# Optimization experiments

Hardware: AMD Instinct MI355X
Metric: run time of the kernel (lower is better)

The kernel has to match this reference:

```python
import jax, jax.numpy as jnp
import numpy as np
import math

B, S, D = 16, 2048, 128
MASK_SENTINEL = -100

def setup_inputs() -> dict:
    key = jax.random.key(0)
    k1, k2, k3, k4 = jax.random.split(key, 4)
    value = jax.random.normal(k1, (B, S, D), dtype=jnp.float32)
    key_t = jax.random.normal(k2, (B, S, D), dtype=jnp.float32)
    query = jax.random.normal(k3, (B, S, D), dtype=jnp.float32)
    # mask uses -100 as the "masked out" sentinel, anything else is kept.
    bits = jax.random.randint(k4, (B, S, S), 0, 2, dtype=jnp.int32)
    mask = jnp.where(bits == 0, jnp.int32(MASK_SENTINEL), jnp.int32(0))
    return {"value": value, "key": key_t, "query": query, "mask": mask}

def reference(value, key, query, mask):
    # scores: [B, Sq, Sk]
    scale = 1.0 / math.sqrt(query.shape[-1])
    scores = jnp.einsum("bqd,bkd->bqk", query, key) * scale
    min_val = jnp.finfo(scores.dtype).min
    masked = jnp.where(mask == MASK_SENTINEL, min_val, scores)
    attn = jax.nn.softmax(masked, axis=-1)
    return jnp.einsum("bqk,bkd->bqd", attn, value)
```

## Files before the change

### kernel.cpp

```cpp
#include <hip/hip_runtime.h>
#include <hip/hip_bf16.h>

#define BATCH 16
#define SEQ   2048
#define DIM   128
#define QBLK  64
#define KVBLK 64
#define NT    (SEQ / KVBLK)
#define PPAD  72
#define L2E   1.4426950408889634f
#define THR   8.0f
#define MSENT -100

typedef __attribute__((ext_vector_type(8))) short bf16x8;
typedef __attribute__((ext_vector_type(4))) float f32x4;
typedef __attribute__((ext_vector_type(4))) int   i32x4;
typedef __attribute__((ext_vector_type(4))) unsigned u32x4;

__device__ __forceinline__ unsigned short f2bf(float f) {
  union { float f; unsigned u; } v; v.f = f;
  return (unsigned short)((v.u + 0x7FFFu + ((v.u >> 16) & 1u)) >> 16);
}
__device__ __forceinline__ unsigned packbf(float a, float b) {
  return ((unsigned)f2bf(b) << 16) | (unsigned)f2bf(a);
}

__global__ __launch_bounds__(256) void cvt_k(const float* __restrict__ K,
                                             short* __restrict__ Kb) {
  const size_t i = ((size_t)blockIdx.x * 256 + threadIdx.x) * 8;
  f32x4 a = __builtin_nontemporal_load((const f32x4*)(K + i));
  f32x4 b = __builtin_nontemporal_load((const f32x4*)(K + i + 4));
  u32x4 o = { packbf(a[0], a[1]), packbf(a[2], a[3]),
              packbf(b[0], b[1]), packbf(b[2], b[3]) };
  *(u32x4*)(Kb + i) = o;
}

__global__ __launch_bounds__(256) void cvt_vt(const float* __restrict__ V,
                                              short* __restrict__ Vt) {
  __shared__ unsigned t32[64][65];
  const int tid = threadIdx.x;
  const int b  = blockIdx.x >> 5;
  const int s0 = (blockIdx.x & 31) * 64;
  #pragma unroll
  for (int it = 0; it < 8; ++it) {
    const int idx = tid + it * 256;
    const int r = idx >> 5, c4 = idx & 31;
    f32x4 x = __builtin_nontemporal_load(
        (const f32x4*)(V + ((size_t)b * SEQ + s0 + r) * DIM + c4 * 4));
    t32[r][c4 * 2]     = packbf(x[0], x[1]);
    t32[r][c4 * 2 + 1] = packbf(x[2], x[3]);
  }
  __syncthreads();
  const int d = tid >> 1, sh = tid & 1;
  unsigned short outv[32];
  #pragma unroll
  for (int j = 0; j < 32; ++j) {
    const unsigned u = t32[sh * 32 + j][d >> 1];
    outv[j] = (d & 1) ? (unsigned short)(u >> 16) : (unsigned short)(u & 0xffff);
  }
  short* op = Vt + ((size_t)b * DIM + d) * SEQ + s0 + sh * 32;
  #pragma unroll
  for (int q = 0; q < 4; ++q) {
    bf16x8 y;
    #pragma unroll
    for (int j = 0; j < 8; ++j) y[j] = (short)outv[q * 8 + j];
    *(bf16x8*)(op + q * 8) = y;
  }
}

__device__ __forceinline__ void gload16(const void* g, void* l) {
  __builtin_amdgcn_global_load_lds(
      (const __attribute__((address_space(1))) unsigned*)g,
      (__attribute__((address_space(3))) unsigned*)l, 16, 0, 0);
}

__device__ __forceinline__ void stage_k(const char* __restrict__ Kb2,
                                        int k0, int w, int l, void* kbuf) {
  #pragma unroll
  for (int it = 0; it < 4; ++it) {
    const int ch = w * 4 + it;
    const int r  = ch * 4 + (l >> 4);
    const int sg = (l & 15) ^ (r & 15);
    gload16(Kb2 + (size_t)(k0 + r) * 256 + sg * 16, (char*)kbuf + ch * 1024);
  }
}
__device__ __forceinline__ void stage_v(const char* __restrict__ Vtb2,
                                        int k0, int w, int l, void* vbuf) {
  #pragma unroll
  for (int it = 0; it < 4; ++it) {
    const int ch = w * 4 + it;
    const int d2 = ch * 4 + (l >> 4);
    const int Su = (l & 15) ^ (d2 & 15);
    const int d  = 2 * d2 + (Su >> 3);
    const int m  = Su & 7;
    gload16(Vtb2 + (size_t)d * (SEQ * 2) + (size_t)k0 * 2 + m * 16,
            (char*)vbuf + ch * 1024);
  }
}

#define TILE_BODY(T, PAR, SA, SB, MA, MB)                                      \
  {                                                                            \
    if ((T) + 2 < NT) stage_k(Kb2, ((T) + 2) * KVBLK, w, l, lds_k[(PAR)]);     \
    if ((T) + 1 < NT) {                                                        \
      stage_v(Vtb2, ((T) + 1) * KVBLK, w, l, lds_v[(PAR) ^ 1]);                \
      _Pragma("unroll") for (int sub = 0; sub < 4; ++sub)                      \
          MB[sub] = __builtin_nontemporal_load(                                \
              (const i32x4*)(Mr + ((T) + 1) * KVBLK + 16 * sub + 4 * g));      \
    }                                                                          \
    __builtin_amdgcn_sched_barrier(0);                                         \
                  \
    _Pragma("unroll") for (int sub = 0; sub < 4; ++sub)                        \
        _Pragma("unroll") for (int i = 0; i < 4; ++i)                          \
            if (MA[sub][i] == MSENT) SA[sub][i] = -1e30f;                      \
    {                                                                          \
      float tm = -1e30f;                                                       \
      _Pragma("unroll") for (int sub = 0; sub < 4; ++sub)                      \
          _Pragma("unroll") for (int i = 0; i < 4; ++i)                        \
              tm = fmaxf(tm, SA[sub][i]);                                      \
      tm = fmaxf(tm, __shfl_xor(tm, 16));                                      \
      tm = fmaxf(tm, __shfl_xor(tm, 32));                                      \
      if (__any(tm > mrow + THR)) {                                            \
        const float mnew = fmaxf(mrow, tm);                                    \
        const float al = __builtin_amdgcn_exp2f((mrow - mnew) * L2E);          \
        mrow = mnew; lsum *= al;                                               \
        float av[4];                                                           \
        _Pragma("unroll") for (int i = 0; i < 4; ++i)                          \
            av[i] = __shfl(al, 4 * g + i);                                     \
        _Pragma("unroll") for (int t8 = 0; t8 < 8; ++t8)                       \
            _Pragma("unroll") for (int i = 0; i < 4; ++i)                      \
                acc[t8][i] *= av[i];                                           \
      }                                                                        \
    }                                                                          \
               \
    if ((T) + 1 < NT) {                                                        \
      const char* kb_ = (const char*)lds_k[(PAR) ^ 1];                         \
      _Pragma("unroll") for (int sub = 0; sub < 4; ++sub)                      \
          SB[sub] = (f32x4){0.f, 0.f, 0.f, 0.f};                               \
      __builtin_amdgcn_s_setprio(1);                                           \
      _Pragma("unroll") for (int kk = 0; kk < 4; ++kk) {                       \
        const int cb = (64 * kk + 16 * g) ^ (lr << 4);                         \
        _Pragma("unroll") for (int sub = 0; sub < 4; ++sub) {                  \
          bf16x8 kb = *(const bf16x8*)(kb_ + (sub * 16 + lr) * 256 + cb);      \
          SB[sub] = __builtin_amdgcn_mfma_f32_16x16x32_bf16(kb, qa[kk],        \
                                                            SB[sub], 0, 0, 0); \
        }                                                                      \
      }                                                                        \
      __builtin_amdgcn_s_setprio(0);                                           \
    }                                                                          \
                               \
    {                                                                          \
      unsigned* prow = (unsigned*)&lds_p[w][lr * PPAD];                        \
      _Pragma("unroll") for (int sub = 0; sub < 4; ++sub) {                    \
        const float p0 = __builtin_amdgcn_exp2f((SA[sub][0] - mrow) * L2E);    \
        const float p1 = __builtin_amdgcn_exp2f((SA[sub][1] - mrow) * L2E);    \
        const float p2 = __builtin_amdgcn_exp2f((SA[sub][2] - mrow) * L2E);    \
        const float p3 = __builtin_amdgcn_exp2f((SA[sub][3] - mrow) * L2E);    \
        lsum += (p0 + p1) + (p2 + p3);                                         \
        prow[8 * sub + 2 * g]     = packbf(p0, p1);                            \
        prow[8 * sub + 2 * g + 1] = packbf(p2, p3);                            \
      }                                                                        \
      bf16x8 pa0 = *(const bf16x8*)&lds_p[w][lr * PPAD + g * 8];               \
      bf16x8 pa1 = *(const bf16x8*)&lds_p[w][lr * PPAD + 32 + g * 8];          \
      const char* vb_ = (const char*)lds_v[(PAR)];                             \
      __builtin_amdgcn_s_setprio(1);                                           \
      _Pragma("unroll") for (int t8 = 0; t8 < 8; ++t8) {                       \
        const int d2 = 8 * t8 + (lr >> 1);                                     \
        const int S0 = (((lr & 1) * 8 + 0 + g) ^ (d2 & 15)) * 16;              \
        const int S1 = (((lr & 1) * 8 + 4 + g) ^ (d2 & 15)) * 16;              \
        bf16x8 v0 = *(const bf16x8*)(vb_ + d2 * 256 + S0);                     \
        acc[t8] = __builtin_amdgcn_mfma_f32_16x16x32_bf16(pa0, v0, acc[t8],    \
                                                          0, 0, 0);            \
        bf16x8 v1 = *(const bf16x8*)(vb_ + d2 * 256 + S1);                     \
        acc[t8] = __builtin_amdgcn_mfma_f32_16x16x32_bf16(pa1, v1, acc[t8],    \
                                                          0, 0, 0);            \
      }                                                                        \
      __builtin_amdgcn_s_setprio(0);                                           \
    }                                                                          \
    if ((T) + 1 < NT) __syncthreads();                                         \
  }

__global__ __launch_bounds__(256, 2) void attn_fwd(
    const short* __restrict__ Kbf, const short* __restrict__ Vt,
    const float* __restrict__ Qg, const int* __restrict__ Mg,
    float* __restrict__ Og) {
  __shared__ short lds_k[2][KVBLK * DIM];
  __shared__ short lds_v[2][DIM * KVBLK];
  __shared__ short lds_p[4][16 * PPAD];

  const int tid = threadIdx.x;
  const int w = tid >> 6, l = tid & 63, g = l >> 4, lr = l & 15;

  const int blk = blockIdx.x;
  const int swz = (blk & 7) * 64 + (blk >> 3);
  const int b   = swz >> 5;
  const int q0  = (swz & 31) * QBLK;

  const float scale = 0.08838834764831845f;

  const char* Kb2  = (const char*)(Kbf + (size_t)b * SEQ * DIM);
  const char* Vtb2 = (const char*)(Vt  + (size_t)b * DIM * SEQ);
  const int*  Mr   = Mg + (size_t)b * SEQ * SEQ + (size_t)(q0 + w * 16 + lr) * SEQ;

  stage_k(Kb2, 0,     w, l, lds_k[0]);
  stage_k(Kb2, KVBLK, w, l, lds_k[1]);
  stage_v(Vtb2, 0,    w, l, lds_v[0]);
  __builtin_amdgcn_sched_barrier(0);
  i32x4 mA[4], mB[4];
  #pragma unroll
  for (int sub = 0; sub < 4; ++sub)
    mA[sub] = __builtin_nontemporal_load((const i32x4*)(Mr + 16 * sub + 4 * g));

  bf16x8 qa[4];
  {
    const float* qbase = Qg + ((size_t)b * SEQ + (size_t)(q0 + w * 16 + lr)) * DIM + g * 8;
    #pragma unroll
    for (int kk = 0; kk < 4; ++kk) {
      f32x4 x0 = *(const f32x4*)(qbase + kk * 32);
      f32x4 x1 = *(const f32x4*)(qbase + kk * 32 + 4);
      bf16x8 f;
      #pragma unroll
      for (int j = 0; j < 4; ++j) {
        f[j]     = (short)f2bf(x0[j] * scale);
        f[j + 4] = (short)f2bf(x1[j] * scale);
      }
      qa[kk] = f;
    }
  }

  f32x4 acc[8];
  #pragma unroll
  for (int t = 0; t < 8; ++t) acc[t] = (f32x4){0.f, 0.f, 0.f, 0.f};
  float mrow = -1e30f, lsum = 0.f;

  __syncthreads();

  f32x4 sA[4], sB[4];
  #pragma unroll
  for (int sub = 0; sub < 4; ++sub) sA[sub] = (f32x4){0.f, 0.f, 0.f, 0.f};
  {
    const char* kb_ = (const char*)lds_k[0];
    #pragma unroll
    for (int kk = 0; kk < 4; ++kk) {
      const int cb = (64 * kk + 16 * g) ^ (lr << 4);
      #pragma unroll
      for (int sub = 0; sub < 4; ++sub) {
        bf16x8 kb = *(const bf16x8*)(kb_ + (sub * 16 + lr) * 256 + cb);
        sA[sub] = __builtin_amdgcn_mfma_f32_16x16x32_bf16(kb, qa[kk], sA[sub], 0, 0, 0);
      }
    }
  }
  __syncthreads();

  for (int t = 0; t < NT; t += 2) {
    TILE_BODY(t,     0, sA, sB, mA, mB);
    TILE_BODY(t + 1, 1, sB, sA, mB, mA);
  }

  lsum += __shfl_xor(lsum, 16);
  lsum += __shfl_xor(lsum, 32);
  const float rden = 1.f / lsum;
  float rdv[4];
  #pragma unroll
  for (int i = 0; i < 4; ++i) rdv[i] = __shfl(rden, 4 * g + i);
  float* ob = Og + ((size_t)b * SEQ + (size_t)(q0 + w * 16)) * DIM;
  #pragma unroll
  for (int t8 = 0; t8 < 8; ++t8)
    #pragma unroll
    for (int i = 0; i < 4; ++i)
      ob[(4 * g + i) * DIM + 16 * t8 + lr] = acc[t8][i] * rdv[i];
}

extern "C" void kernel_launch(void* const* d_in, const int* in_sizes, int n_in,
                              void* d_out, int out_size, void* d_ws, size_t ws_size,
                              hipStream_t stream) {
  (void)in_sizes; (void)n_in; (void)out_size; (void)ws_size;
  const float* Vg = (const float*)d_in[0];
  const float* Kg = (const float*)d_in[1];
  const float* Qg = (const float*)d_in[2];
  const int*   Mg = (const int*)d_in[3];
  float* Og = (float*)d_out;

  short* Kbf = (short*)d_ws;
  short* Vt  = Kbf + (size_t)BATCH * SEQ * DIM;
  cvt_k<<<dim3(BATCH * SEQ * DIM / (8 * 256)), 256, 0, stream>>>(Kg, Kbf);
  cvt_vt<<<dim3(BATCH * (SEQ / 64)), 256, 0, stream>>>(Vg, Vt);
  attn_fwd<<<dim3(BATCH * (SEQ / QBLK)), 256, 0, stream>>>(Kbf, Vt, Qg, Mg, Og);
}
```

Measured before the change: 109.0 us.

## Shrink KV tile to 32, triple-buffer K/V, pass P via shuffles instead of LDS

```diff
diff --git a/kernel.cpp b/kernel.cpp
--- a/kernel.cpp
+++ b/kernel.cpp
@@ -5,9 +5,8 @@
 #define SEQ   2048
 #define DIM   128
 #define QBLK  64
-#define KVBLK 64
-#define NT    (SEQ / KVBLK)
-#define PPAD  72
+#define KVB   32
+#define NT    (SEQ / KVB)
 #define L2E   1.4426950408889634f
 #define THR   8.0f
 #define MSENT -100
@@ -74,49 +73,47 @@
       (__attribute__((address_space(3))) unsigned*)l, 16, 0, 0);
 }
 
-__device__ __forceinline__ void stage_k(const char* __restrict__ Kb2,
-                                        int k0, int w, int l, void* kbuf) {
-  #pragma unroll
-  for (int it = 0; it < 4; ++it) {
-    const int ch = w * 4 + it;
+__device__ __forceinline__ void stage_k32(const char* __restrict__ Kb2,
+                                          int k0, int w, int l, void* kbuf) {
+  #pragma unroll
+  for (int it = 0; it < 2; ++it) {
+    const int ch = w * 2 + it;
     const int r  = ch * 4 + (l >> 4);
     const int sg = (l & 15) ^ (r & 15);
     gload16(Kb2 + (size_t)(k0 + r) * 256 + sg * 16, (char*)kbuf + ch * 1024);
   }
 }
-__device__ __forceinline__ void stage_v(const char* __restrict__ Vtb2,
-                                        int k0, int w, int l, void* vbuf) {
-  #pragma unroll
-  for (int it = 0; it < 4; ++it) {
-    const int ch = w * 4 + it;
-    const int d2 = ch * 4 + (l >> 4);
-    const int Su = (l & 15) ^ (d2 & 15);
-    const int d  = 2 * d2 + (Su >> 3);
-    const int m  = Su & 7;
-    gload16(Vtb2 + (size_t)d * (SEQ * 2) + (size_t)k0 * 2 + m * 16,
+__device__ __forceinline__ void stage_v32(const char* __restrict__ Vtb2,
+                                          int k0, int w, int l, void* vbuf) {
+  #pragma unroll
+  for (int it = 0; it < 2; ++it) {
+    const int ch = w * 2 + it;
+    const int d  = ch * 16 + (l >> 2);
+    const int sp = (l & 3) ^ ((l >> 3) & 3);
+    gload16(Vtb2 + (size_t)d * (SEQ * 2) + (size_t)k0 * 2 + sp * 16,
             (char*)vbuf + ch * 1024);
   }
 }
 
-#define TILE_BODY(T, PAR, SA, SB, MA, MB)                                      \
+#define TILE_BODY(T, SA, SB, MA, MB, BARMODE)                                  \
   {                                                                            \
-    if ((T) + 2 < NT) stage_k(Kb2, ((T) + 2) * KVBLK, w, l, lds_k[(PAR)]);     \
+    if ((T) + 3 < NT) stage_k32(Kb2, ((T) + 3) * KVB, w, l, kA);               \
+    if ((T) + 2 < NT) stage_v32(Vtb2, ((T) + 2) * KVB, w, l, vC);              \
     if ((T) + 1 < NT) {                                                        \
-      stage_v(Vtb2, ((T) + 1) * KVBLK, w, l, lds_v[(PAR) ^ 1]);                \
-      _Pragma("unroll") for (int sub = 0; sub < 4; ++sub)                      \
-          MB[sub] = __builtin_nontemporal_load(                                \
-              (const i32x4*)(Mr + ((T) + 1) * KVBLK + 16 * sub + 4 * g));      \
+      MB[0] = __builtin_nontemporal_load(                                      \
+          (const i32x4*)(Mr + ((T) + 1) * KVB + 4 * g));                       \
+      MB[1] = __builtin_nontemporal_load(                                      \
+          (const i32x4*)(Mr + ((T) + 1) * KVB + 16 + 4 * g));                  \
     }                                                                          \
     __builtin_amdgcn_sched_barrier(0);                                         \
                   \
-    _Pragma("unroll") for (int sub = 0; sub < 4; ++sub)                        \
+    _Pragma("unroll") for (int sub = 0; sub < 2; ++sub)                        \
         _Pragma("unroll") for (int i = 0; i < 4; ++i)                          \
             if (MA[sub][i] == MSENT) SA[sub][i] = -1e30f;                      \
     {                                                                          \
-      float tm = -1e30f;                                                       \
-      _Pragma("unroll") for (int sub = 0; sub < 4; ++sub)                      \
-          _Pragma("unroll") for (int i = 0; i < 4; ++i)                        \
-              tm = fmaxf(tm, SA[sub][i]);                                      \
+      float tm = fmaxf(fmaxf(SA[0][0], SA[0][1]), fmaxf(SA[0][2], SA[0][3])); \
+      tm = fmaxf(tm, fmaxf(fmaxf(SA[1][0], SA[1][1]),                          \
+                           fmaxf(SA[1][2], SA[1][3])));                        \
       tm = fmaxf(tm, __shfl_xor(tm, 16));                                      \
       tm = fmaxf(tm, __shfl_xor(tm, 32));                                      \
       if (__any(tm > mrow + THR)) {                                            \
@@ -131,61 +128,76 @@
                 acc[t8][i] *= av[i];                                           \
       }                                                                        \
     }                                                                          \
-               \
+                       \
     if ((T) + 1 < NT) {                                                        \
-      const char* kb_ = (const char*)lds_k[(PAR) ^ 1];                         \
-      _Pragma("unroll") for (int sub = 0; sub < 4; ++sub)                      \
-          SB[sub] = (f32x4){0.f, 0.f, 0.f, 0.f};                               \
+      SB[0] = (f32x4){0.f, 0.f, 0.f, 0.f};                                     \
+      SB[1] = (f32x4){0.f, 0.f, 0.f, 0.f};                                     \
       __builtin_amdgcn_s_setprio(1);                                           \
       _Pragma("unroll") for (int kk = 0; kk < 4; ++kk) {                       \
         const int cb = (64 * kk + 16 * g) ^ (lr << 4);                         \
-        _Pragma("unroll") for (int sub = 0; sub < 4; ++sub) {                  \
-          bf16x8 kb = *(const bf16x8*)(kb_ + (sub * 16 + lr) * 256 + cb);      \
-          SB[sub] = __builtin_amdgcn_mfma_f32_16x16x32_bf16(kb, qa[kk],        \
-                                                            SB[sub], 0, 0, 0); \
-        }                                                                      \
+        bf16x8 kb0 = *(const bf16x8*)(kB + lr * 256 + cb);                     \
+        bf16x8 kb1 = *(const bf16x8*)(kB + (16 + lr) * 256 + cb);              \
+        SB[0] = __builtin_amdgcn_mfma_f32_16x16x32_bf16(kb0, qa[kk], SB[0],    \
+                                                        0, 0, 0);              \
+        SB[1] = __builtin_amdgcn_mfma_f32_16x16x32_bf16(kb1, qa[kk], SB[1],    \
+                                                        0, 0, 0);              \
       }                                                                        \
       __builtin_amdgcn_s_setprio(0);                                           \
     }                                                                          \
-                               \
+      \
     {                                                                          \
-      unsigned* prow = (unsigned*)&lds_p[w][lr * PPAD];                        \
-      _Pragma("unroll") for (int sub = 0; sub < 4; ++sub) {                    \
+      unsigned pk[2][2];                                                       \
+      _Pragma("unroll") for (int sub = 0; sub < 2; ++sub) {                    \
         const float p0 = __builtin_amdgcn_exp2f((SA[sub][0] - mrow) * L2E);    \
         const float p1 = __builtin_amdgcn_exp2f((SA[sub][1] - mrow) * L2E);    \
         const float p2 = __builtin_amdgcn_exp2f((SA[sub][2] - mrow) * L2E);    \
         const float p3 = __builtin_amdgcn_exp2f((SA[sub][3] - mrow) * L2E);    \
         lsum += (p0 + p1) + (p2 + p3);                                         \
-        prow[8 * sub + 2 * g]     = packbf(p0, p1);                            \
-        prow[8 * sub + 2 * g + 1] = packbf(p2, p3);                            \
-      }                                                                        \
-      bf16x8 pa0 = *(const bf16x8*)&lds_p[w][lr * PPAD + g * 8];               \
-      bf16x8 pa1 = *(const bf16x8*)&lds_p[w][lr * PPAD + 32 + g * 8];          \
-      const char* vb_ = (const char*)lds_v[(PAR)];                             \
+        pk[sub][0] = packbf(p0, p1);                                           \
+        pk[sub][1] = packbf(p2, p3);                                           \
+      }                                                                        \
+      const unsigned s00 = (unsigned)__shfl((int)pk[0][0], laneA);             \
+      const unsigned s01 = (unsigned)__shfl((int)pk[0][1], laneA);             \
+      const unsigned s02 = (unsigned)__shfl((int)pk[0][0], laneB);             \
+      const unsigned s03 = (unsigned)__shfl((int)pk[0][1], laneB);             \
+      const unsigned s10 = (unsigned)__shfl((int)pk[1][0], laneA);             \
+      const unsigned s11 = (unsigned)__shfl((int)pk[1][1], laneA);             \
+      const unsigned s12 = (unsigned)__shfl((int)pk[1][0], laneB);             \
+      const unsigned s13 = (unsigned)__shfl((int)pk[1][1], laneB);             \
+      const bool hi = (g >= 2);                                                \
+      union { unsigned u[4]; bf16x8 v; } pa;                                   \
+      pa.u[0] = hi ? s10 : s00;                                                \
+      pa.u[1] = hi ? s11 : s01;                                                \
+      pa.u[2] = hi ? s12 : s02;                                                \
+      pa.u[3] = hi ? s13 : s03;                                                \
+      const int Sv = ((g ^ ((lr >> 1) & 3)) << 4);                             \
       __builtin_amdgcn_s_setprio(1);                                           \
       _Pragma("unroll") for (int t8 = 0; t8 < 8; ++t8) {                       \
-        const int d2 = 8 * t8 + (lr >> 1);                                     \
-        const int S0 = (((lr & 1) * 8 + 0 + g) ^ (d2 & 15)) * 16;              \
-        const int S1 = (((lr & 1) * 8 + 4 + g) ^ (d2 & 15)) * 16;              \
-        bf16x8 v0 = *(const bf16x8*)(vb_ + d2 * 256 + S0);                     \
-        acc[t8] = __builtin_amdgcn_mfma_f32_16x16x32_bf16(pa0, v0, acc[t8],    \
+        bf16x8 vb = *(const bf16x8*)(vA + (16 * t8 + lr) * 64 + Sv);           \
+        acc[t8] = __builtin_amdgcn_mfma_f32_16x16x32_bf16(pa.v, vb, acc[t8],   \
                                                           0, 0, 0);            \
-        bf16x8 v1 = *(const bf16x8*)(vb_ + d2 * 256 + S1);                     \
-        acc[t8] = __builtin_amdgcn_mfma_f32_16x16x32_bf16(pa1, v1, acc[t8],    \
-                                                          0, 0, 0);            \
       }                                                                        \
       __builtin_amdgcn_s_setprio(0);                                           \
     }                                                                          \
-    if ((T) + 1 < NT) __syncthreads();                                         \
+    if ((T) + 1 < NT) {                                                        \
+      if (BARMODE) {                                                           \
+        __syncthreads();                                                       \
+      } else {                                                                 \
+        asm volatile("s_waitcnt vmcnt(6)" ::: "memory");                       \
+        __builtin_amdgcn_s_barrier();                                          \
+        __builtin_amdgcn_sched_barrier(0);                                     \
+      }                                                                        \
+    }                                                                          \
+    { char* t_ = kA; kA = kB; kB = kC; kC = t_; }                              \
+    { char* t_ = vA; vA = vB; vB = vC; vC = t_; }                              \
   }
 
 __global__ __launch_bounds__(256, 2) void attn_fwd(
     const short* __restrict__ Kbf, const short* __restrict__ Vt,
     const float* __restrict__ Qg, const int* __restrict__ Mg,
     float* __restrict__ Og) {
-  __shared__ short lds_k[2][KVBLK * DIM];
-  __shared__ short lds_v[2][DIM * KVBLK];
-  __shared__ short lds_p[4][16 * PPAD];
+  __shared__ short lds_k[3][KVB * DIM];
+  __shared__ short lds_v[3][DIM * KVB];
 
   const int tid = threadIdx.x;
   const int w = tid >> 6, l = tid & 63, g = l >> 4, lr = l & 15;
@@ -201,14 +213,18 @@
   const char* Vtb2 = (const char*)(Vt  + (size_t)b * DIM * SEQ);
   const int*  Mr   = Mg + (size_t)b * SEQ * SEQ + (size_t)(q0 + w * 16 + lr) * SEQ;
 
-  stage_k(Kb2, 0,     w, l, lds_k[0]);
-  stage_k(Kb2, KVBLK, w, l, lds_k[1]);
-  stage_v(Vtb2, 0,    w, l, lds_v[0]);
+  char *kA = (char*)lds_k[0], *kB = (char*)lds_k[1], *kC = (char*)lds_k[2];
+  char *vA = (char*)lds_v[0], *vB = (char*)lds_v[1], *vC = (char*)lds_v[2];
+
+  stage_k32(Kb2, 0,       w, l, kA);
+  stage_k32(Kb2, KVB,     w, l, kB);
+  stage_k32(Kb2, 2 * KVB, w, l, kC);
+  stage_v32(Vtb2, 0,      w, l, vA);
+  stage_v32(Vtb2, KVB,    w, l, vB);
   __builtin_amdgcn_sched_barrier(0);
-  i32x4 mA[4], mB[4];
-  #pragma unroll
-  for (int sub = 0; sub < 4; ++sub)
-    mA[sub] = __builtin_nontemporal_load((const i32x4*)(Mr + 16 * sub + 4 * g));
+  i32x4 mA[2], mB[2];
+  mA[0] = __builtin_nontemporal_load((const i32x4*)(Mr + 4 * g));
+  mA[1] = __builtin_nontemporal_load((const i32x4*)(Mr + 16 + 4 * g));
 
   bf16x8 qa[4];
   {
@@ -232,29 +248,32 @@
   for (int t = 0; t < 8; ++t) acc[t] = (f32x4){0.f, 0.f, 0.f, 0.f};
   float mrow = -1e30f, lsum = 0.f;
 
+  const int laneA = ((g & 1) << 5) + lr;
+  const int laneB = laneA + 16;
+
   __syncthreads();
 
-  f32x4 sA[4], sB[4];
-  #pragma unroll
-  for (int sub = 0; sub < 4; ++sub) sA[sub] = (f32x4){0.f, 0.f, 0.f, 0.f};
-  {
-    const char* kb_ = (const char*)lds_k[0];
-    #pragma unroll
-    for (int kk = 0; kk < 4; ++kk) {
-      const int cb = (64 * kk + 16 * g) ^ (lr << 4);
-      #pragma unroll
-      for (int sub = 0; sub < 4; ++sub) {
-        bf16x8 kb = *(const bf16x8*)(kb_ + (sub * 16 + lr) * 256 + cb);
-        sA[sub] = __builtin_amdgcn_mfma_f32_16x16x32_bf16(kb, qa[kk], sA[sub], 0, 0, 0);
-      }
-    }
+  f32x4 sA[2], sB[2];
+  sA[0] = (f32x4){0.f, 0.f, 0.f, 0.f};
+  sA[1] = (f32x4){0.f, 0.f, 0.f, 0.f};
+  #pragma unroll
+  for (int kk = 0; kk < 4; ++kk) {
+    const int cb = (64 * kk + 16 * g) ^ (lr << 4);
+    bf16x8 kb0 = *(const bf16x8*)(kA + lr * 256 + cb);
+    bf16x8 kb1 = *(const bf16x8*)(kA + (16 + lr) * 256 + cb);
+    sA[0] = __builtin_amdgcn_mfma_f32_16x16x32_bf16(kb0, qa[kk], sA[0], 0, 0, 0);
+    sA[1] = __builtin_amdgcn_mfma_f32_16x16x32_bf16(kb1, qa[kk], sA[1], 0, 0, 0);
   }
   __syncthreads();
 
-  for (int t = 0; t < NT; t += 2) {
-    TILE_BODY(t,     0, sA, sB, mA, mB);
-    TILE_BODY(t + 1, 1, sB, sA, mB, mA);
-  }
+  for (int t = 0; t < 60; t += 2) {
+    TILE_BODY(t,     sA, sB, mA, mB, 0);
+    TILE_BODY(t + 1, sB, sA, mB, mA, 0);
+  }
+  TILE_BODY(60, sA, sB, mA, mB, 1);
+  TILE_BODY(61, sB, sA, mB, mA, 1);
+  TILE_BODY(62, sA, sB, mA, mB, 1);
+  TILE_BODY(63, sB, sA, mB, mA, 1);
 
   lsum += __shfl_xor(lsum, 16);
   lsum += __shfl_xor(lsum, 32);
```

After: 124.0 us. +13.7%, slower.
